# Optimization experiments

Hardware: AMD Instinct MI355X
Metric: run time of the kernel (lower is better)

Reference implementation:

```python
import jax, jax.numpy as jnp
import numpy as np
import math

HEADS = 16
NEG_FILL = -9e15
LN_EPS = 1e-6


def setup_inputs() -> dict:
    key = jax.random.key(0)
    ks = jax.random.split(key, 7)
    B, S, D = 8, 1024, 1024
    x = jax.random.normal(ks[0], (B, S, D), dtype=jnp.float32)
    mask = jax.random.randint(ks[1], (B, S), 0, 2).astype(bool)
    # ensure at least one valid key position per row
    mask = mask.at[:, 0].set(True)
    scale = 0.02
    Wq = jax.random.normal(ks[2], (D, D), dtype=jnp.float32) * scale  # torch Linear weight [out,in]
    Wk = jax.random.normal(ks[3], (D, D), dtype=jnp.float32) * scale
    Wv = jax.random.normal(ks[4], (D, D), dtype=jnp.float32) * scale
    gamma = jnp.ones((D,), dtype=jnp.float32)
    beta = jnp.zeros((D,), dtype=jnp.float32)
    return {"x": x, "mask": mask, "Wq": Wq, "Wk": Wk, "Wv": Wv, "gamma": gamma, "beta": beta}


def reference(x, mask, Wq, Wk, Wv, gamma, beta):
    B, S, D = x.shape
    H = HEADS
    dk = D // H
    # Linear(d, d, bias=False): y = x @ W.T; split heads -> [B,H,S,dk]
    def proj(W):
        return jnp.einsum('bsd,ed->bse', x, W).reshape(B, S, H, dk).transpose(0, 2, 1, 3)
    q, k, v = proj(Wq), proj(Wk), proj(Wv)
    scores = jnp.einsum('bhqd,bhkd->bhqk', q, k) / math.sqrt(dk)
    # mask broadcast: key-padding mask over keys, same for all queries/heads
    scores = jnp.where(mask[:, None, None, :], scores, NEG_FILL)
    attn = jax.nn.softmax(scores, axis=-1)  # dropout is identity in eval
    out = jnp.einsum('bhqk,bhkd->bhqd', attn, v)
    out = out.transpose(0, 2, 1, 3).reshape(B, S, D) + x  # residual
    # LayerNorm(eps=1e-6) over last dim
    mu = jnp.mean(out, axis=-1, keepdims=True)
    var = jnp.mean(jnp.square(out - mu), axis=-1, keepdims=True)
    out = (out - mu) * jax.lax.rsqrt(var + LN_EPS) * gamma + beta
    return attn, out
```

## Files before the change

kernel.cpp:

```cpp
#include <hip/hip_runtime.h>

typedef __bf16 bf16x8 __attribute__((ext_vector_type(8)));
typedef float f32x4 __attribute__((ext_vector_type(4)));
typedef unsigned short ushort_t;
typedef unsigned char uchar_t;

#define MFMA_16x16x32(A, B, C) __builtin_amdgcn_mfma_f32_16x16x32_bf16(A, B, C, 0, 0, 0)

__device__ __forceinline__ float bf2f(ushort_t u) {
  unsigned int x = ((unsigned int)u) << 16;
  float f;
  __builtin_memcpy(&f, &x, 4);
  return f;
}
__device__ __forceinline__ ushort_t f2bf(float f) {
  unsigned int x;
  __builtin_memcpy(&x, &f, 4);
  x = x + 0x7fffu + ((x >> 16) & 1u);
  return (ushort_t)(x >> 16);
}
__device__ __forceinline__ ushort_t f2bf_s(float f) {
  if (!(__builtin_fabsf(f) < 3.0e38f)) f = 0.0f;
  return f2bf(f);
}

__device__ __forceinline__ void gload_lds16(const void* g, void* l) {
  __builtin_amdgcn_global_load_lds(
      (__attribute__((address_space(1))) void*)const_cast<void*>(g),
      (__attribute__((address_space(3))) void*)l, 16, 0, 0);
}

__device__ __forceinline__ uint4 cvt8(float4 a, float4 b) {
  uint4 r;
  r.x = (unsigned)f2bf_s(a.x) | ((unsigned)f2bf_s(a.y) << 16);
  r.y = (unsigned)f2bf_s(a.z) | ((unsigned)f2bf_s(a.w) << 16);
  r.z = (unsigned)f2bf_s(b.x) | ((unsigned)f2bf_s(b.y) << 16);
  r.w = (unsigned)f2bf_s(b.z) | ((unsigned)f2bf_s(b.w) << 16);
  return r;
}

__device__ __forceinline__ int sci32(int r, int col) {
  int g = col >> 3;
  g = (g & ~7) | ((g ^ r) & 7);
  return (r << 10) + (g << 3) + (col & 7);
}

__launch_bounds__(256)
__global__ void cvt_f32_bf16(const float* __restrict__ in, ushort_t* __restrict__ out, int n4) {
  int i = blockIdx.x * 256 + threadIdx.x;
  if (i >= n4) return;
  float4 v = ((const float4*)in)[i];
  ushort4 r;
  r.x = f2bf_s(v.x);
  r.y = f2bf_s(v.y);
  r.z = f2bf_s(v.z);
  r.w = f2bf_s(v.w);
  ((ushort4*)out)[i] = r;
}

template <bool SCATTER>
__launch_bounds__(256)
__global__ void gemm_bt(const ushort_t* __restrict__ A, const ushort_t* __restrict__ B,
                        ushort_t* __restrict__ C) {
  constexpr int BK = 32, LD = 1024, K = 1024;
  constexpr int WM = 64, WN = 64, MR = 4, NR = 4;

  __shared__ ushort_t lA[128 * BK];
  __shared__ ushort_t lB[128 * BK];

  const int m0 = blockIdx.y * 128;
  const int n0 = blockIdx.x * 128;
  const int tid = threadIdx.x;
  const int lane = tid & 63, wid = tid >> 6;
  const int wr = wid >> 1, wc = wid & 1;

  f32x4 acc[MR][NR] = {};

  for (int k0 = 0; k0 < K; k0 += BK) {
#pragma unroll
    for (int i = 0; i < 2; ++i) {
      int idx = i * 256 + tid;
      const ushort_t* g = A + (long long)(m0 + (idx >> 2)) * LD + k0 + (idx & 3) * 8;
      gload_lds16(g, (void*)(lA + (i * 256 + wid * 64) * 8));
    }
#pragma unroll
    for (int i = 0; i < 2; ++i) {
      int idx = i * 256 + tid;
      const ushort_t* g = B + (long long)(n0 + (idx >> 2)) * LD + k0 + (idx & 3) * 8;
      gload_lds16(g, (void*)(lB + (i * 256 + wid * 64) * 8));
    }
    __syncthreads();

    bf16x8 af[MR], bf[NR];
#pragma unroll
    for (int m = 0; m < MR; ++m)
      af[m] = *(const bf16x8*)&lA[(wr * WM + m * 16 + (lane & 15)) * BK + (lane >> 4) * 8];
#pragma unroll
    for (int n = 0; n < NR; ++n)
      bf[n] = *(const bf16x8*)&lB[(wc * WN + n * 16 + (lane & 15)) * BK + (lane >> 4) * 8];
#pragma unroll
    for (int m = 0; m < MR; ++m)
#pragma unroll
      for (int n = 0; n < NR; ++n)
        acc[m][n] = MFMA_16x16x32(af[m], bf[n], acc[m][n]);
    __syncthreads();
  }

  if constexpr (!SCATTER) {
#pragma unroll
    for (int m = 0; m < MR; ++m)
#pragma unroll
      for (int n = 0; n < NR; ++n)
#pragma unroll
        for (int j = 0; j < 4; ++j) {
          int row = m0 + wr * WM + m * 16 + (lane >> 4) * 4 + j;
          int col = n0 + wc * WN + n * 16 + (lane & 15);
          C[(long long)row * LD + col] = f2bf(acc[m][n][j]);
        }
  } else {
#pragma unroll
    for (int m = 0; m < MR; ++m)
#pragma unroll
      for (int n = 0; n < NR; ++n) {
        int row = m0 + wr * WM + m * 16 + (lane >> 4) * 4;
        int col = n0 + wc * WN + n * 16 + (lane & 15);
        int b = row >> 10, s = row & 1023;
        int h = col >> 6, dk = col & 63;
        ushort4 pk;
        pk.x = f2bf(acc[m][n][0]);
        pk.y = f2bf(acc[m][n][1]);
        pk.z = f2bf(acc[m][n][2]);
        pk.w = f2bf(acc[m][n][3]);
        *(ushort4*)(C + ((long long)(b * 16 + h)) * 65536 + (long long)dk * 1024 + s) = pk;
      }
  }
}

__launch_bounds__(256)
__global__ void gemm_proj(const float* __restrict__ A, const float* __restrict__ B,
                          ushort_t* __restrict__ C, int K, int lda, int ldb, int ldc) {
  constexpr int BM = 128, BN = 128, BK = 32;
  constexpr int WM = 64, WN = 64, MR = 4, NR = 4;
  __shared__ ushort_t lA[BM * BK];
  __shared__ ushort_t lB[BN * BK];
  const int m0 = blockIdx.y * BM, n0 = blockIdx.x * BN;
  const int tid = threadIdx.x, lane = tid & 63, wid = tid >> 6;
  const int wr = wid >> 1, wc = wid & 1;
  f32x4 acc[MR][NR] = {};
  for (int k0 = 0; k0 < K; k0 += BK) {
#pragma unroll
    for (int i = 0; i < 2; ++i) {
      int idx = i * 256 + tid;
      const float* g = A + (long long)(m0 + (idx >> 2)) * lda + k0 + (idx & 3) * 8;
      *(uint4*)&lA[idx * 8] = cvt8(*(const float4*)g, *(const float4*)(g + 4));
    }
#pragma unroll
    for (int i = 0; i < 2; ++i) {
      int idx = i * 256 + tid;
      const float* g = B + (long long)(n0 + (idx >> 2)) * ldb + k0 + (idx & 3) * 8;
      *(uint4*)&lB[idx * 8] = cvt8(*(const float4*)g, *(const float4*)(g + 4));
    }
    __syncthreads();
    bf16x8 af[MR], bf[NR];
#pragma unroll
    for (int m = 0; m < MR; ++m)
      af[m] = *(const bf16x8*)&lA[(wr * WM + m * 16 + (lane & 15)) * BK + (lane >> 4) * 8];
#pragma unroll
    for (int n = 0; n < NR; ++n)
      bf[n] = *(const bf16x8*)&lB[(wc * WN + n * 16 + (lane & 15)) * BK + (lane >> 4) * 8];
#pragma unroll
    for (int m = 0; m < MR; ++m)
#pragma unroll
      for (int n = 0; n < NR; ++n)
        acc[m][n] = MFMA_16x16x32(af[m], bf[n], acc[m][n]);
    __syncthreads();
  }
#pragma unroll
  for (int m = 0; m < MR; ++m)
#pragma unroll
    for (int n = 0; n < NR; ++n)
#pragma unroll
      for (int j = 0; j < 4; ++j) {
        int row = m0 + wr * WM + m * 16 + (lane >> 4) * 4 + j;
        int col = n0 + wc * WN + n * 16 + (lane & 15);
        C[(long long)row * ldc + col] = f2bf(acc[m][n][j]);
      }
}

__launch_bounds__(256)
__global__ void gemm_vt(const float* __restrict__ A, const float* __restrict__ B,
                        ushort_t* __restrict__ Vt) {
  constexpr int BM = 128, BN = 128, BK = 32, D = 1024;
  constexpr int WM = 64, WN = 64, MR = 4, NR = 4;
  __shared__ ushort_t lA[BM * BK];
  __shared__ ushort_t lB[BN * BK];
  const int m0 = blockIdx.y * BM, n0 = blockIdx.x * BN;
  const int tid = threadIdx.x, lane = tid & 63, wid = tid >> 6;
  const int wr = wid >> 1, wc = wid & 1;
  f32x4 acc[MR][NR] = {};
  for (int k0 = 0; k0 < D; k0 += BK) {
#pragma unroll
    for (int i = 0; i < 2; ++i) {
      int idx = i * 256 + tid;
      const float* g = A + (long long)(m0 + (idx >> 2)) * D + k0 + (idx & 3) * 8;
      *(uint4*)&lA[idx * 8] = cvt8(*(const float4*)g, *(const float4*)(g + 4));
    }
#pragma unroll
    for (int i = 0; i < 2; ++i) {
      int idx = i * 256 + tid;
      const float* g = B + (long long)(n0 + (idx >> 2)) * D + k0 + (idx & 3) * 8;
      *(uint4*)&lB[idx * 8] = cvt8(*(const float4*)g, *(const float4*)(g + 4));
    }
    __syncthreads();
    bf16x8 af[MR], bf[NR];
#pragma unroll
    for (int m = 0; m < MR; ++m)
      af[m] = *(const bf16x8*)&lA[(wr * WM + m * 16 + (lane & 15)) * BK + (lane >> 4) * 8];
#pragma unroll
    for (int n = 0; n < NR; ++n)
      bf[n] = *(const bf16x8*)&lB[(wc * WN + n * 16 + (lane & 15)) * BK + (lane >> 4) * 8];
#pragma unroll
    for (int m = 0; m < MR; ++m)
#pragma unroll
      for (int n = 0; n < NR; ++n)
        acc[m][n] = MFMA_16x16x32(af[m], bf[n], acc[m][n]);
    __syncthreads();
  }
#pragma unroll
  for (int m = 0; m < MR; ++m)
#pragma unroll
    for (int n = 0; n < NR; ++n) {
      int row = m0 + wr * WM + m * 16 + (lane >> 4) * 4;
      int col = n0 + wc * WN + n * 16 + (lane & 15);
      int b = row >> 10, s = row & 1023;
      int h = col >> 6, dk = col & 63;
      ushort4 pk;
      pk.x = f2bf(acc[m][n][0]);
      pk.y = f2bf(acc[m][n][1]);
      pk.z = f2bf(acc[m][n][2]);
      pk.w = f2bf(acc[m][n][3]);
      *(ushort4*)(Vt + ((long long)(b * 16 + h)) * 65536 + (long long)dk * 1024 + s) = pk;
    }
}

__launch_bounds__(512, 4)
__global__ void fused_attn(const ushort_t* __restrict__ Qp, const ushort_t* __restrict__ Kp,
                           const ushort_t* __restrict__ Vt, const int* __restrict__ mask,
                           float* __restrict__ attn, float* __restrict__ out) {
  constexpr int S = 1024, D = 1024;
  __shared__ ushort_t sc[32 * 1024];
  __shared__ float red[2048];
  __shared__ float inv_s[32];
  __shared__ uchar_t ms[1024];

  const int n = blockIdx.x;
  const int xcd = n & 7, s8 = n >> 3;
  const int bh = xcd + 8 * (s8 >> 5);
  const int q0 = (s8 & 31) * 32;
  const int b = bh >> 4, h = bh & 15;
  const int t = threadIdx.x, lane = t & 63, w = t >> 6;

  if (t < 256) {
    int4 mv = ((const int4*)(mask + b * S))[t];
    ms[t * 4 + 0] = (uchar_t)mv.x;
    ms[t * 4 + 1] = (uchar_t)mv.y;
    ms[t * 4 + 2] = (uchar_t)mv.z;
    ms[t * 4 + 3] = (uchar_t)mv.w;
  }

  bf16x8 qa00, qa01, qa10, qa11;
  {
    const ushort_t* q =
        Qp + ((long long)(b * S + q0 + (lane & 15))) * D + h * 64 + (lane >> 4) * 8;
    qa00 = *(const bf16x8*)q;
    qa01 = *(const bf16x8*)(q + 32);
    qa10 = *(const bf16x8*)(q + 16 * D);
    qa11 = *(const bf16x8*)(q + 16 * D + 32);
  }
  __syncthreads();

  {
    const ushort_t* kfb =
        Kp + ((long long)(b * S + w * 16 + (lane & 15))) * D + h * 64 + (lane >> 4) * 8;
#pragma unroll
    for (int kb = 0; kb < 8; ++kb) {
      const ushort_t* g = kfb + (long long)kb * 128 * D;
      bf16x8 kf0 = *(const bf16x8*)g;
      bf16x8 kf1 = *(const bf16x8*)(g + 32);
      f32x4 a0 = {}, a1 = {};
      a0 = MFMA_16x16x32(qa00, kf0, a0);
      a0 = MFMA_16x16x32(qa01, kf1, a0);
      a1 = MFMA_16x16x32(qa10, kf0, a1);
      a1 = MFMA_16x16x32(qa11, kf1, a1);
      int key = kb * 128 + w * 16 + (lane & 15);
      bool valid = ms[key] != 0;
#pragma unroll
      for (int j = 0; j < 4; ++j) {
        int r = (lane >> 4) * 4 + j;
        sc[sci32(r, key)] = f2bf(valid ? a0[j] * 0.125f : -30000.0f);
        sc[sci32(16 + r, key)] = f2bf(valid ? a1[j] * 0.125f : -30000.0f);
      }
    }
  }
  __syncthreads();

  {
    const int r = t >> 4, c = t & 15;
    float m = -3.0e38f;
#pragma unroll
    for (int i = 0; i < 16; ++i) {
      ushort4 sv = *(const ushort4*)&sc[sci32(r, c * 4 + i * 64)];
      m = fmaxf(m, fmaxf(fmaxf(bf2f(sv.x), bf2f(sv.y)), fmaxf(bf2f(sv.z), bf2f(sv.w))));
    }
#pragma unroll
    for (int off = 8; off; off >>= 1) m = fmaxf(m, __shfl_xor(m, off, 64));

    float sum = 0.f;
#pragma unroll
    for (int i = 0; i < 16; ++i) {
      int idx = sci32(r, c * 4 + i * 64);
      ushort4 sv = *(const ushort4*)&sc[idx];
      float p0 = __expf(bf2f(sv.x) - m);
      float p1 = __expf(bf2f(sv.y) - m);
      float p2 = __expf(bf2f(sv.z) - m);
      float p3 = __expf(bf2f(sv.w) - m);
      sum += (p0 + p1) + (p2 + p3);
      ushort4 pv;
      pv.x = f2bf(p0);
      pv.y = f2bf(p1);
      pv.z = f2bf(p2);
      pv.w = f2bf(p3);
      *(ushort4*)&sc[idx] = pv;
    }
#pragma unroll
    for (int off = 8; off; off >>= 1) sum += __shfl_xor(sum, off, 64);
    float inv = 1.0f / sum;
    if (c == 0) inv_s[r] = inv;

    float* arow = attn + ((long long)bh << 20) + ((long long)(q0 + r) << 10);
#pragma unroll
    for (int i = 0; i < 16; ++i) {
      ushort4 pv = *(const ushort4*)&sc[sci32(r, c * 4 + i * 64)];
      float4 o;
      o.x = bf2f(pv.x) * inv;
      o.y = bf2f(pv.y) * inv;
      o.z = bf2f(pv.z) * inv;
      o.w = bf2f(pv.w) * inv;
      *(float4*)&arow[c * 4 + i * 64] = o;
    }
  }
  __syncthreads();

  {
    const int dq = w & 3, kh = w >> 2;
    f32x4 acc0 = {}, acc1 = {};
    const ushort_t* vfb = Vt + ((long long)bh << 16) +
                          ((long long)(dq * 16 + (lane & 15)) << 10) + kh * 512 +
                          (lane >> 4) * 8;
#pragma unroll
    for (int kc = 0; kc < 16; ++kc) {
      bf16x8 vb = *(const bf16x8*)(vfb + kc * 32);
      int kslice = kh * 512 + kc * 32 + (lane >> 4) * 8;
      bf16x8 p0 = *(const bf16x8*)&sc[sci32(lane & 15, kslice)];
      bf16x8 p1 = *(const bf16x8*)&sc[sci32(16 + (lane & 15), kslice)];
      acc0 = MFMA_16x16x32(p0, vb, acc0);
      acc1 = MFMA_16x16x32(p1, vb, acc1);
    }
    if (kh == 1) {
      *(f32x4*)&red[((dq * 2 + 0) * 64 + lane) * 4] = acc0;
      *(f32x4*)&red[((dq * 2 + 1) * 64 + lane) * 4] = acc1;
    }
    __syncthreads();
    if (kh == 0) {
      f32x4 o0 = *(const f32x4*)&red[((dq * 2 + 0) * 64 + lane) * 4];
      f32x4 o1 = *(const f32x4*)&red[((dq * 2 + 1) * 64 + lane) * 4];
      float* ob = out + ((long long)b << 20) + ((long long)q0 << 10) + h * 64 + dq * 16 +
                  (lane & 15);
#pragma unroll
      for (int j = 0; j < 4; ++j) {
        int r0 = (lane >> 4) * 4 + j;
        int r1 = 16 + r0;
        ob[(long long)r0 << 10] = (acc0[j] + o0[j]) * inv_s[r0];
        ob[(long long)r1 << 10] = (acc1[j] + o1[j]) * inv_s[r1];
      }
    }
  }
}

__launch_bounds__(256)
__global__ void attn_scores(const ushort_t* __restrict__ Qp, const ushort_t* __restrict__ Kp,
                            const int* __restrict__ mask, float* __restrict__ attn) {
  constexpr int S = 1024, D = 1024;
  __shared__ float scl[16][1028];
  __shared__ ushort_t ktl[64][72];
  const int q0 = blockIdx.x * 16;
  const int bh = blockIdx.y, b = bh >> 4, h = bh & 15;
  const int tid = threadIdx.x, lane = tid & 63, wid = tid >> 6;
  bf16x8 qa0, qa1;
  {
    const ushort_t* q =
        Qp + ((long long)(b * S + q0 + (lane & 15))) * D + h * 64 + (lane >> 4) * 8;
    qa0 = *(const bf16x8*)q;
    qa1 = *(const bf16x8*)(q + 32);
  }
  for (int kb = 0; kb < 16; ++kb) {
    {
      int r = tid >> 2, cg = (tid & 3) * 16;
      const ushort_t* g = Kp + ((long long)(b * S + kb * 64 + r)) * D + h * 64 + cg;
      *(uint4*)&ktl[r][cg] = *(const uint4*)g;
      *(uint4*)&ktl[r][cg + 8] = *(const uint4*)(g + 8);
    }
    __syncthreads();
    {
      int krow = wid * 16 + (lane & 15);
      bf16x8 b0 = *(const bf16x8*)&ktl[krow][(lane >> 4) * 8];
      bf16x8 b1 = *(const bf16x8*)&ktl[krow][32 + (lane >> 4) * 8];
      f32x4 acc = {};
      acc = MFMA_16x16x32(qa0, b0, acc);
      acc = MFMA_16x16x32(qa1, b1, acc);
      int key = kb * 64 + wid * 16 + (lane & 15);
      int mv = mask[b * S + key];
#pragma unroll
      for (int j = 0; j < 4; ++j)
        scl[(lane >> 4) * 4 + j][key] = mv ? acc[j] * 0.125f : -30000.0f;
    }
    __syncthreads();
  }
  for (int rr = 0; rr < 4; ++rr) {
    int r = wid * 4 + rr;
    float v[16];
    float mx = -3.0e38f;
#pragma unroll
    for (int i = 0; i < 16; ++i) {
      v[i] = scl[r][lane + i * 64];
      mx = fmaxf(mx, v[i]);
    }
#pragma unroll
    for (int off = 32; off; off >>= 1) mx = fmaxf(mx, __shfl_xor(mx, off, 64));
    float sum = 0.f;
#pragma unroll
    for (int i = 0; i < 16; ++i) {
      v[i] = __expf(v[i] - mx);
      sum += v[i];
    }
#pragma unroll
    for (int off = 32; off; off >>= 1) sum += __shfl_xor(sum, off, 64);
    float inv = 1.0f / sum;
    float* o = attn + (long long)bh * S * S + (long long)(q0 + r) * S + lane;
#pragma unroll
    for (int i = 0; i < 16; ++i) o[i * 64] = v[i] * inv;
  }
}

__launch_bounds__(256)
__global__ void gemm_pv(const float* __restrict__ attn, const ushort_t* __restrict__ Vt,
                        float* __restrict__ out) {
  constexpr int S = 1024, D = 1024;
  constexpr int BM = 128, BK = 32;
  constexpr int WM = 64, WN = 32, MR = 4, NR = 2;
  __shared__ ushort_t lA[BM * BK];
  __shared__ ushort_t lB[64 * BK];
  const int bh = blockIdx.z, b = bh >> 4, h = bh & 15;
  const float* A = attn + (long long)bh * S * S;
  const ushort_t* B = Vt + (long long)bh * 65536;
  float* C = out + (long long)b * S * D + h * 64;
  const int m0 = blockIdx.y * BM;
  const int tid = threadIdx.x, lane = tid & 63, wid = tid >> 6;
  const int wr = wid >> 1, wc = wid & 1;
  f32x4 acc[MR][NR] = {};
  for (int k0 = 0; k0 < S; k0 += BK) {
#pragma unroll
    for (int i = 0; i < 2; ++i) {
      int idx = i * 256 + tid;
      const float* g = A + (long long)(m0 + (idx >> 2)) * S + k0 + (idx & 3) * 8;
      *(uint4*)&lA[idx * 8] = cvt8(*(const float4*)g, *(const float4*)(g + 4));
    }
    {
      int row = tid >> 2, cg = (tid & 3) * 8;
      *(uint4*)&lB[row * BK + cg] = *(const uint4*)(B + (long long)row * S + k0 + cg);
    }
    __syncthreads();
    bf16x8 af[MR], bf[NR];
#pragma unroll
    for (int m = 0; m < MR; ++m)
      af[m] = *(const bf16x8*)&lA[(wr * WM + m * 16 + (lane & 15)) * BK + (lane >> 4) * 8];
#pragma unroll
    for (int n = 0; n < NR; ++n)
      bf[n] = *(const bf16x8*)&lB[(wc * WN + n * 16 + (lane & 15)) * BK + (lane >> 4) * 8];
#pragma unroll
    for (int m = 0; m < MR; ++m)
#pragma unroll
      for (int n = 0; n < NR; ++n)
        acc[m][n] = MFMA_16x16x32(af[m], bf[n], acc[m][n]);
    __syncthreads();
  }
#pragma unroll
  for (int m = 0; m < MR; ++m)
#pragma unroll
    for (int n = 0; n < NR; ++n)
#pragma unroll
      for (int j = 0; j < 4; ++j) {
        int row = m0 + wr * WM + m * 16 + (lane >> 4) * 4 + j;
        int col = wc * WN + n * 16 + (lane & 15);
        C[(long long)row * D + col] = acc[m][n][j];
      }
}

__launch_bounds__(256)
__global__ void ln_residual(const float* __restrict__ x, const float* __restrict__ gamma,
                            const float* __restrict__ beta, float* __restrict__ out) {
  constexpr int D = 1024;
  __shared__ float red[8];
  const int row = blockIdx.x;
  const int tid = threadIdx.x, lane = tid & 63, wid = tid >> 6;
  const int d0 = tid * 4;
  float4 xv = *(const float4*)(x + (long long)row * D + d0);
  float4 ov = *(const float4*)(out + (long long)row * D + d0);
  float v[4];
  v[0] = xv.x + ov.x;
  v[1] = xv.y + ov.y;
  v[2] = xv.z + ov.z;
  v[3] = xv.w + ov.w;
  float sum = v[0] + v[1] + v[2] + v[3];
  float sq = v[0] * v[0] + v[1] * v[1] + v[2] * v[2] + v[3] * v[3];
#pragma unroll
  for (int off = 32; off; off >>= 1) {
    sum += __shfl_xor(sum, off, 64);
    sq += __shfl_xor(sq, off, 64);
  }
  if (lane == 0) {
    red[wid] = sum;
    red[4 + wid] = sq;
  }
  __syncthreads();
  sum = red[0] + red[1] + red[2] + red[3];
  sq = red[4] + red[5] + red[6] + red[7];
  const float mu = sum * (1.0f / 1024.0f);
  const float var = sq * (1.0f / 1024.0f) - mu * mu;
  const float rs = rsqrtf(var + 1e-6f);
  float4 gv = *(const float4*)(gamma + d0);
  float4 bv = *(const float4*)(beta + d0);
  float4 r;
  r.x = (v[0] - mu) * rs * gv.x + bv.x;
  r.y = (v[1] - mu) * rs * gv.y + bv.y;
  r.z = (v[2] - mu) * rs * gv.z + bv.z;
  r.w = (v[3] - mu) * rs * gv.w + bv.w;
  *(float4*)(out + (long long)row * D + d0) = r;
}

extern "C" void kernel_launch(void* const* d_in, const int* in_sizes, int n_in,
                              void* d_out, int out_size, void* d_ws, size_t ws_size,
                              hipStream_t stream) {
  const int B = 8, S = 1024, D = 1024, H = 16;
  const float* x = (const float*)d_in[0];
  const int* mask = (const int*)d_in[1];
  const float* Wq = (const float*)d_in[2];
  const float* Wk = (const float*)d_in[3];
  const float* Wv = (const float*)d_in[4];
  const float* gamma = (const float*)d_in[5];
  const float* beta = (const float*)d_in[6];

  float* attn = (float*)d_out;
  float* out = attn + (long long)B * H * S * S;

  const long long BSD = (long long)B * S * D;
  const long long DDe = (long long)D * D;
  const size_t MB = 1u << 20;
  ushort_t* ws = (ushort_t*)d_ws;

  if (ws_size >= 70 * MB) {
    ushort_t* xb = ws;
    ushort_t* Wqb = xb + BSD;
    ushort_t* Wkb = Wqb + DDe;
    ushort_t* Wvb = Wkb + DDe;
    ushort_t* Qp = Wvb + DDe;
    ushort_t* Kp = Qp + BSD;
    ushort_t* Vt = Kp + BSD;
    cvt_f32_bf16<<<dim3((int)(BSD / 4 / 256)), 256, 0, stream>>>(x, xb, (int)(BSD / 4));
    cvt_f32_bf16<<<dim3((int)(DDe / 4 / 256)), 256, 0, stream>>>(Wq, Wqb, (int)(DDe / 4));
    cvt_f32_bf16<<<dim3((int)(DDe / 4 / 256)), 256, 0, stream>>>(Wk, Wkb, (int)(DDe / 4));
    cvt_f32_bf16<<<dim3((int)(DDe / 4 / 256)), 256, 0, stream>>>(Wv, Wvb, (int)(DDe / 4));
    gemm_bt<false><<<dim3(D / 128, (B * S) / 128), 256, 0, stream>>>(xb, Wqb, Qp);
    gemm_bt<false><<<dim3(D / 128, (B * S) / 128), 256, 0, stream>>>(xb, Wkb, Kp);
    gemm_bt<true><<<dim3(D / 128, (B * S) / 128), 256, 0, stream>>>(xb, Wvb, Vt);
    fused_attn<<<dim3((S / 32) * B * H), 512, 0, stream>>>(Qp, Kp, Vt, mask, attn, out);
    ln_residual<<<dim3(B * S), 256, 0, stream>>>(x, gamma, beta, out);
  } else if (ws_size >= 48 * MB) {
    ushort_t* Qp = ws;
    ushort_t* Kp = Qp + BSD;
    ushort_t* Vt = Kp + BSD;
    gemm_proj<<<dim3(D / 128, (B * S) / 128), 256, 0, stream>>>(x, Wq, Qp, D, D, D, D);
    gemm_proj<<<dim3(D / 128, (B * S) / 128), 256, 0, stream>>>(x, Wk, Kp, D, D, D, D);
    gemm_vt<<<dim3(D / 128, (B * S) / 128), 256, 0, stream>>>(x, Wv, Vt);
    fused_attn<<<dim3((S / 32) * B * H), 512, 0, stream>>>(Qp, Kp, Vt, mask, attn, out);
    ln_residual<<<dim3(B * S), 256, 0, stream>>>(x, gamma, beta, out);
  } else {
    ushort_t* Qp = ws;
    ushort_t* Kp = Qp + BSD;
    ushort_t* Vt = Qp;
    gemm_proj<<<dim3(D / 128, (B * S) / 128), 256, 0, stream>>>(x, Wq, Qp, D, D, D, D);
    gemm_proj<<<dim3(D / 128, (B * S) / 128), 256, 0, stream>>>(x, Wk, Kp, D, D, D, D);
    attn_scores<<<dim3(S / 16, B * H), 256, 0, stream>>>(Qp, Kp, mask, attn);
    gemm_vt<<<dim3(D / 128, (B * S) / 128), 256, 0, stream>>>(x, Wv, Vt);
    gemm_pv<<<dim3(1, S / 128, B * H), 256, 0, stream>>>(attn, Vt, out);
    ln_residual<<<dim3(B * S), 256, 0, stream>>>(x, gamma, beta, out);
  }
}
```

Baseline: 355.5 us.

## Shrink fused attention tile to 16 queries per 256-thread block

The fused attention kernel now handles 16 query rows per 256-thread block instead of 32 rows per 512 threads. This halves shared memory use and removes the split-key cross-wave reduction buffer and its extra barrier in the PV stage, so more blocks can reside per CU. The normalized attention-probability write moves after the barrier and is reorganized so each wave writes whole rows with contiguous lanes. In exchange, K and V tiles are reloaded from global memory twice as often, since each block covers fewer queries.

```diff
diff --git a/kernel.cpp b/kernel.cpp
--- a/kernel.cpp
+++ b/kernel.cpp
@@ -243,24 +243,23 @@
     }
 }
 
-__launch_bounds__(512, 4)
+__launch_bounds__(256, 4)
 __global__ void fused_attn(const ushort_t* __restrict__ Qp, const ushort_t* __restrict__ Kp,
                            const ushort_t* __restrict__ Vt, const int* __restrict__ mask,
                            float* __restrict__ attn, float* __restrict__ out) {
   constexpr int S = 1024, D = 1024;
-  __shared__ ushort_t sc[32 * 1024];
-  __shared__ float red[2048];
-  __shared__ float inv_s[32];
+  __shared__ ushort_t sc[16 * 1024];
+  __shared__ float inv_s[16];
   __shared__ uchar_t ms[1024];
 
   const int n = blockIdx.x;
   const int xcd = n & 7, s8 = n >> 3;
-  const int bh = xcd + 8 * (s8 >> 5);
-  const int q0 = (s8 & 31) * 32;
+  const int bh = xcd + 8 * (s8 >> 6);
+  const int q0 = (s8 & 63) * 16;
   const int b = bh >> 4, h = bh & 15;
   const int t = threadIdx.x, lane = t & 63, w = t >> 6;
 
-  if (t < 256) {
+  {
     int4 mv = ((const int4*)(mask + b * S))[t];
     ms[t * 4 + 0] = (uchar_t)mv.x;
     ms[t * 4 + 1] = (uchar_t)mv.y;
@@ -268,14 +267,12 @@
     ms[t * 4 + 3] = (uchar_t)mv.w;
   }
 
-  bf16x8 qa00, qa01, qa10, qa11;
+  bf16x8 qa0, qa1;
   {
     const ushort_t* q =
         Qp + ((long long)(b * S + q0 + (lane & 15))) * D + h * 64 + (lane >> 4) * 8;
-    qa00 = *(const bf16x8*)q;
-    qa01 = *(const bf16x8*)(q + 32);
-    qa10 = *(const bf16x8*)(q + 16 * D);
-    qa11 = *(const bf16x8*)(q + 16 * D + 32);
+    qa0 = *(const bf16x8*)q;
+    qa1 = *(const bf16x8*)(q + 32);
   }
   __syncthreads();
 
@@ -283,23 +280,18 @@
     const ushort_t* kfb =
         Kp + ((long long)(b * S + w * 16 + (lane & 15))) * D + h * 64 + (lane >> 4) * 8;
 #pragma unroll
-    for (int kb = 0; kb < 8; ++kb) {
-      const ushort_t* g = kfb + (long long)kb * 128 * D;
+    for (int kb = 0; kb < 16; ++kb) {
+      const ushort_t* g = kfb + (long long)kb * 64 * D;
       bf16x8 kf0 = *(const bf16x8*)g;
       bf16x8 kf1 = *(const bf16x8*)(g + 32);
-      f32x4 a0 = {}, a1 = {};
-      a0 = MFMA_16x16x32(qa00, kf0, a0);
-      a0 = MFMA_16x16x32(qa01, kf1, a0);
-      a1 = MFMA_16x16x32(qa10, kf0, a1);
-      a1 = MFMA_16x16x32(qa11, kf1, a1);
-      int key = kb * 128 + w * 16 + (lane & 15);
+      f32x4 a0 = {};
+      a0 = MFMA_16x16x32(qa0, kf0, a0);
+      a0 = MFMA_16x16x32(qa1, kf1, a0);
+      int key = kb * 64 + w * 16 + (lane & 15);
       bool valid = ms[key] != 0;
 #pragma unroll
-      for (int j = 0; j < 4; ++j) {
-        int r = (lane >> 4) * 4 + j;
-        sc[sci32(r, key)] = f2bf(valid ? a0[j] * 0.125f : -30000.0f);
-        sc[sci32(16 + r, key)] = f2bf(valid ? a1[j] * 0.125f : -30000.0f);
-      }
+      for (int j = 0; j < 4; ++j)
+        sc[sci32((lane >> 4) * 4 + j, key)] = f2bf(valid ? a0[j] * 0.125f : -30000.0f);
     }
   }
   __syncthreads();
@@ -334,55 +326,45 @@
     }
 #pragma unroll
     for (int off = 8; off; off >>= 1) sum += __shfl_xor(sum, off, 64);
-    float inv = 1.0f / sum;
-    if (c == 0) inv_s[r] = inv;
-
-    float* arow = attn + ((long long)bh << 20) + ((long long)(q0 + r) << 10);
-#pragma unroll
-    for (int i = 0; i < 16; ++i) {
-      ushort4 pv = *(const ushort4*)&sc[sci32(r, c * 4 + i * 64)];
-      float4 o;
-      o.x = bf2f(pv.x) * inv;
-      o.y = bf2f(pv.y) * inv;
-      o.z = bf2f(pv.z) * inv;
-      o.w = bf2f(pv.w) * inv;
-      *(float4*)&arow[c * 4 + i * 64] = o;
-    }
+    if (c == 0) inv_s[r] = 1.0f / sum;
   }
   __syncthreads();
 
   {
-    const int dq = w & 3, kh = w >> 2;
-    f32x4 acc0 = {}, acc1 = {};
+    float* abase = attn + ((long long)bh << 20) + ((long long)q0 << 10);
+#pragma unroll
+    for (int rr = 0; rr < 4; ++rr) {
+      int r = w * 4 + rr;
+      float inv = inv_s[r];
+#pragma unroll
+      for (int i = 0; i < 4; ++i) {
+        int col = lane * 4 + i * 256;
+        ushort4 pv = *(const ushort4*)&sc[sci32(r, col)];
+        float4 o;
+        o.x = bf2f(pv.x) * inv;
+        o.y = bf2f(pv.y) * inv;
+        o.z = bf2f(pv.z) * inv;
+        o.w = bf2f(pv.w) * inv;
+        *(float4*)&abase[((long long)r << 10) + col] = o;
+      }
+    }
+
+    const int dq = w;
+    f32x4 acc = {};
     const ushort_t* vfb = Vt + ((long long)bh << 16) +
-                          ((long long)(dq * 16 + (lane & 15)) << 10) + kh * 512 +
-                          (lane >> 4) * 8;
-#pragma unroll
-    for (int kc = 0; kc < 16; ++kc) {
+                          ((long long)(dq * 16 + (lane & 15)) << 10) + (lane >> 4) * 8;
+#pragma unroll
+    for (int kc = 0; kc < 32; ++kc) {
       bf16x8 vb = *(const bf16x8*)(vfb + kc * 32);
-      int kslice = kh * 512 + kc * 32 + (lane >> 4) * 8;
-      bf16x8 p0 = *(const bf16x8*)&sc[sci32(lane & 15, kslice)];
-      bf16x8 p1 = *(const bf16x8*)&sc[sci32(16 + (lane & 15), kslice)];
-      acc0 = MFMA_16x16x32(p0, vb, acc0);
-      acc1 = MFMA_16x16x32(p1, vb, acc1);
-    }
-    if (kh == 1) {
-      *(f32x4*)&red[((dq * 2 + 0) * 64 + lane) * 4] = acc0;
-      *(f32x4*)&red[((dq * 2 + 1) * 64 + lane) * 4] = acc1;
-    }
-    __syncthreads();
-    if (kh == 0) {
-      f32x4 o0 = *(const f32x4*)&red[((dq * 2 + 0) * 64 + lane) * 4];
-      f32x4 o1 = *(const f32x4*)&red[((dq * 2 + 1) * 64 + lane) * 4];
-      float* ob = out + ((long long)b << 20) + ((long long)q0 << 10) + h * 64 + dq * 16 +
-                  (lane & 15);
-#pragma unroll
-      for (int j = 0; j < 4; ++j) {
-        int r0 = (lane >> 4) * 4 + j;
-        int r1 = 16 + r0;
-        ob[(long long)r0 << 10] = (acc0[j] + o0[j]) * inv_s[r0];
-        ob[(long long)r1 << 10] = (acc1[j] + o1[j]) * inv_s[r1];
-      }
+      bf16x8 p0 = *(const bf16x8*)&sc[sci32(lane & 15, kc * 32 + (lane >> 4) * 8)];
+      acc = MFMA_16x16x32(p0, vb, acc);
+    }
+    float* ob = out + ((long long)b << 20) + ((long long)q0 << 10) + h * 64 + dq * 16 +
+                (lane & 15);
+#pragma unroll
+    for (int j = 0; j < 4; ++j) {
+      int r = (lane >> 4) * 4 + j;
+      ob[(long long)r << 10] = acc[j] * inv_s[r];
     }
   }
 }
@@ -583,7 +565,7 @@
     gemm_bt<false><<<dim3(D / 128, (B * S) / 128), 256, 0, stream>>>(xb, Wqb, Qp);
     gemm_bt<false><<<dim3(D / 128, (B * S) / 128), 256, 0, stream>>>(xb, Wkb, Kp);
     gemm_bt<true><<<dim3(D / 128, (B * S) / 128), 256, 0, stream>>>(xb, Wvb, Vt);
-    fused_attn<<<dim3((S / 32) * B * H), 512, 0, stream>>>(Qp, Kp, Vt, mask, attn, out);
+    fused_attn<<<dim3((S / 16) * B * H), 256, 0, stream>>>(Qp, Kp, Vt, mask, attn, out);
     ln_residual<<<dim3(B * S), 256, 0, stream>>>(x, gamma, beta, out);
   } else if (ws_size >= 48 * MB) {
     ushort_t* Qp = ws;
@@ -592,7 +574,7 @@
     gemm_proj<<<dim3(D / 128, (B * S) / 128), 256, 0, stream>>>(x, Wq, Qp, D, D, D, D);
     gemm_proj<<<dim3(D / 128, (B * S) / 128), 256, 0, stream>>>(x, Wk, Kp, D, D, D, D);
     gemm_vt<<<dim3(D / 128, (B * S) / 128), 256, 0, stream>>>(x, Wv, Vt);
-    fused_attn<<<dim3((S / 32) * B * H), 512, 0, stream>>>(Qp, Kp, Vt, mask, attn, out);
+    fused_attn<<<dim3((S / 16) * B * H), 256, 0, stream>>>(Qp, Kp, Vt, mask, attn, out);
     ln_residual<<<dim3(B * S), 256, 0, stream>>>(x, gamma, beta, out);
   } else {
     ushort_t* Qp = ws;
```

Result: slower. 431.9 us (+21.5%).
